# Kernel tuning notes

Hardware: AMD Instinct MI355X
Metric: run time of the kernel (lower is better)

## Reference

```python
import jax, jax.numpy as jnp
import numpy as np

B, N, C, H = 4, 2048, 384, 8
HD = C // H  # 48; divisible by 6 so RoPE3D splits into three even-sized chunks
ROPE_BASE = 100.0  # RoPE3D(100)


def _rope1d(x, p):
    # x: [B,H,N,d], p: [B,N] integer positions
    d = x.shape[-1]
    inv = 1.0 / (ROPE_BASE ** (jnp.arange(0, d, 2, dtype=jnp.float32) / d))  # [d/2]
    ang = p[:, None, :, None].astype(jnp.float32) * inv                      # [B,1,N,d/2]
    ang = jnp.concatenate([ang, ang], axis=-1)                               # [B,1,N,d]
    cos, sin = jnp.cos(ang), jnp.sin(ang)
    x1, x2 = jnp.split(x, 2, axis=-1)
    return x * cos + jnp.concatenate([-x2, x1], axis=-1) * sin


def _rope3d(x, pos):
    # x: [B,H,N,D], pos: [B,N,3]; rotate each D/3 chunk by one spatial axis
    parts = jnp.split(x, 3, axis=-1)
    return jnp.concatenate([_rope1d(parts[i], pos[..., i]) for i in range(3)], axis=-1)


def setup_inputs() -> dict:
    key = jax.random.key(0)
    ks = jax.random.split(key, 9)
    T = B * N
    s = 1.0 / np.sqrt(C).astype(np.float32)
    offs = jnp.arange(1, B + 1, dtype=jnp.int32) * N  # equal-length segments
    return {
        "query": jax.random.normal(ks[0], (T, C), jnp.float32),
        "key": jax.random.normal(ks[1], (T, C), jnp.float32),
        "value": jax.random.normal(ks[2], (T, C), jnp.float32),
        "Wq": jax.random.normal(ks[3], (C, C), jnp.float32) * s,
        "bq": jnp.zeros((C,), jnp.float32),
        "Wk": jax.random.normal(ks[4], (C, C), jnp.float32) * s,
        "bk": jnp.zeros((C,), jnp.float32),
        "Wv": jax.random.normal(ks[5], (C, C), jnp.float32) * s,
        "bv": jnp.zeros((C,), jnp.float32),
        "Wo": jax.random.normal(ks[6], (C, C), jnp.float32) * s,
        "bo": jnp.zeros((C,), jnp.float32),
        "qpos": jax.random.randint(ks[7], (T, 3), 0, 100),
        "kpos": jax.random.randint(ks[8], (T, 3), 0, 100),
        "src_point_offset": offs,
        "tgt_point_offset": offs,
    }


def reference(query, key, value, Wq, bq, Wk, bk, Wv, bv, Wo, bo,
              qpos, kpos, src_point_offset, tgt_point_offset):
    # Equal-length segments (offsets = [N,2N,...]) => the per-item python loop
    # in forward_pcd_to_pcd is exactly one batched attention over [B,N,C].
    qb = query.reshape(B, N, C)
    kb = key.reshape(B, N, C)
    vb = value.reshape(B, N, C)
    q = (qb @ Wq.T + bq).reshape(B, N, H, HD).transpose(0, 2, 1, 3)  # [B,H,N,HD]
    k = (kb @ Wk.T + bk).reshape(B, N, H, HD).transpose(0, 2, 1, 3)
    v = (vb @ Wv.T + bv).reshape(B, N, H, HD).transpose(0, 2, 1, 3)
    q = _rope3d(q, qpos.reshape(B, N, 3))
    k = _rope3d(k, kpos.reshape(B, N, 3))
    scale = 1.0 / np.sqrt(HD).astype(np.float32)
    attn = jax.nn.softmax(jnp.einsum("bhqd,bhkd->bhqk", q, k) * scale, axis=-1)
    x = jnp.einsum("bhqk,bhkd->bhqd", attn, v)  # [B,H,N,HD]
    x = x.transpose(0, 2, 1, 3).reshape(B * N, C)
    return x @ Wo.T + bo
```

## Files before the change

### kernel.cpp

```cpp
#include <hip/hip_runtime.h>
#include <hip/hip_bf16.h>
#include <math.h>


typedef __attribute__((ext_vector_type(8))) short bf16x8;
typedef __attribute__((ext_vector_type(4))) float f32x4;
typedef __attribute__((ext_vector_type(4))) short s16x4;

__device__ inline short f2bf(float f) {
    unsigned u = __float_as_uint(f);
    u += 0x7fffu + ((u >> 16) & 1u);
    return (short)(u >> 16);
}
__device__ inline unsigned pk_bf16(float a, float b) {
    __hip_bfloat162 h = __float22bfloat162_rn(make_float2(a, b));
    return *(reinterpret_cast<unsigned*>(&h));
}
__device__ inline unsigned pk2(float lo, float hi) {
    return (__float_as_uint(lo) >> 16) | (__float_as_uint(hi) & 0xffff0000u);
}
__device__ inline float bflo(unsigned u) { return __uint_as_float(u << 16); }
__device__ inline float bfhi(unsigned u) { return __uint_as_float(u & 0xffff0000u); }
__device__ inline float exp2f_fast(float x) {
#if __has_builtin(__builtin_amdgcn_exp2f)
    return __builtin_amdgcn_exp2f(x);
#else
    return exp2f(x);
#endif
}
__device__ inline float ffract(float x) {
    float r;
    asm("v_fract_f32 %0, %1" : "=v"(r) : "v"(x));
    return r;
}
__device__ inline float fsin(float x) {
    float r;
    asm("v_sin_f32 %0, %1\n\ts_nop 1" : "=v"(r) : "v"(x));
    return r;
}
__device__ inline float fcos(float x) {
    float r;
    asm("v_cos_f32 %0, %1\n\ts_nop 1" : "=v"(r) : "v"(x));
    return r;
}
__device__ inline int div48(int c) { return (c * 683) >> 15; }

__global__ __launch_bounds__(256)
void cvt_w(const float* __restrict__ w0, const float* __restrict__ w1,
           const float* __restrict__ w2, const float* __restrict__ w3,
           short* __restrict__ Wh, short* __restrict__ Wl)
{
    const float* s = blockIdx.y == 0 ? w0 : blockIdx.y == 1 ? w1
                   : blockIdx.y == 2 ? w2 : w3;
    const size_t base = (size_t)blockIdx.y * 147456;
    const size_t i = (size_t)(blockIdx.x * 256 + threadIdx.x) * 4;
    const float4 x = *(const float4*)(s + i);
    const unsigned h01 = pk2(x.x, x.y);
    const unsigned h23 = pk2(x.z, x.w);
    uint2 hv; hv.x = h01; hv.y = h23;
    uint2 lv;
    lv.x = pk2(x.x - bflo(h01), x.y - bfhi(h01));
    lv.y = pk2(x.z - bflo(h23), x.w - bfhi(h23));
    *(uint2*)(Wh + base + i) = hv;
    *(uint2*)(Wl + base + i) = lv;
}

__global__ __launch_bounds__(256)
void gemm_qkv(const float* __restrict__ q_in, const float* __restrict__ k_in,
              const float* __restrict__ v_in,
              const short* __restrict__ Whp, const short* __restrict__ Wlp,
              const float* __restrict__ bq, const float* __restrict__ bk,
              const float* __restrict__ bv,
              const int* __restrict__ qpos, const int* __restrict__ kpos,
              short* __restrict__ qp0, short* __restrict__ qtb,
              short* __restrict__ kp0, short* __restrict__ ktb,
              short* __restrict__ vp)
{
    __shared__ short Wls[2][128 * 40];

    const int z = blockIdx.z;
    const float* A = z == 0 ? q_in : z == 1 ? k_in : v_in;
    const short* Wh = Whp + (size_t)z * 147456;
    const short* Wl = Wlp + (size_t)z * 147456;
    const float* bias = z == 0 ? bq : z == 1 ? bk : bv;

    const int tid = threadIdx.x;
    const int wv = tid >> 6, lane = tid & 63;
    const int l15 = lane & 15, quad = lane >> 4;
    const int mb = blockIdx.x * 64 + (wv & 1) * 32;
    const int nbl = (wv >> 1) * 64;
    const int n0 = blockIdx.y * 128;

    const int srow = tid >> 1;
    const int sh = (tid & 1) * 16;
    const short* wg_h = Wh + (size_t)(n0 + srow) * 384 + sh;
    const short* wg_l = Wl + (size_t)(n0 + srow) * 384 + sh;
    short* ds_h = &Wls[0][srow * 40 + sh];
    short* ds_l = &Wls[1][srow * 40 + sh];

    f32x4 acc[2][4] = {};
    const float* a0 = A + (size_t)(mb + l15) * 384 + quad * 8;

    for (int ks = 0; ks < 12; ++ks) {
        const int o = ks * 32;
        __syncthreads();
        *(bf16x8*)(ds_h)     = *(const bf16x8*)(wg_h + o);
        *(bf16x8*)(ds_h + 8) = *(const bf16x8*)(wg_h + o + 8);
        *(bf16x8*)(ds_l)     = *(const bf16x8*)(wg_l + o);
        *(bf16x8*)(ds_l + 8) = *(const bf16x8*)(wg_l + o + 8);
        bf16x8 ah[2], al[2];
        #pragma unroll
        for (int mt = 0; mt < 2; ++mt) {
            const float4 x0 = *(const float4*)(a0 + o + mt * 16 * 384);
            const float4 x1 = *(const float4*)(a0 + o + mt * 16 * 384 + 4);
            union { bf16x8 v; unsigned u[4]; } ch, cl;
            ch.u[0] = pk2(x0.x, x0.y);
            ch.u[1] = pk2(x0.z, x0.w);
            ch.u[2] = pk2(x1.x, x1.y);
            ch.u[3] = pk2(x1.z, x1.w);
            cl.u[0] = pk2(x0.x - bflo(ch.u[0]), x0.y - bfhi(ch.u[0]));
            cl.u[1] = pk2(x0.z - bflo(ch.u[1]), x0.w - bfhi(ch.u[1]));
            cl.u[2] = pk2(x1.x - bflo(ch.u[2]), x1.y - bfhi(ch.u[2]));
            cl.u[3] = pk2(x1.z - bflo(ch.u[3]), x1.w - bfhi(ch.u[3]));
            ah[mt] = ch.v;
            al[mt] = cl.v;
        }
        __syncthreads();

        #pragma unroll
        for (int nt = 0; nt < 4; ++nt) {
            const int wr = (nbl + nt * 16 + l15) * 40 + quad * 8;
            const bf16x8 wh = *(const bf16x8*)&Wls[0][wr];
            const bf16x8 wl = *(const bf16x8*)&Wls[1][wr];
            #pragma unroll
            for (int mt = 0; mt < 2; ++mt) {
                acc[mt][nt] = __builtin_amdgcn_mfma_f32_16x16x32_bf16(
                    ah[mt], wh, acc[mt][nt], 0, 0, 0);
                acc[mt][nt] = __builtin_amdgcn_mfma_f32_16x16x32_bf16(
                    al[mt], wh, acc[mt][nt], 0, 0, 0);
                acc[mt][nt] = __builtin_amdgcn_mfma_f32_16x16x32_bf16(
                    ah[mt], wl, acc[mt][nt], 0, 0, 0);
            }
        }
    }

    if (z < 2) {
        const int* pos = z ? kpos : qpos;
        const float oscale = z ? 1.0f : 0.2082339551542919f;
        const float invf = exp2f_fast(-(float)(l15 & 7) * 0.8304820237218405f)
                         * 0.15915494309189535f;
        const bool lo_half = (l15 < 8);
        #pragma unroll
        for (int nt = 0; nt < 4; ++nt) {
            const int c = n0 + nbl + nt * 16 + l15;
            const int h = div48(c);
            const int r0 = c - h * 48;
            const int axis = r0 >> 4;
            const float bb = bias[c];
            #pragma unroll
            for (int mt = 0; mt < 2; ++mt) {
                float a[4], pr[4];
                #pragma unroll
                for (int r = 0; r < 4; ++r) a[r] = acc[mt][nt][r] + bb;
                #pragma unroll
                for (int r = 0; r < 4; ++r) pr[r] = __shfl_xor(a[r], 8);
                #pragma unroll
                for (int r = 0; r < 4; ++r) {
                    const int t = mb + mt * 16 + quad * 4 + r;
                    const float pp = (float)pos[t * 3 + axis];
                    const float fr = ffract(pp * invf);
                    const float sn = fsin(fr), cn = fcos(fr);
                    const float o2 = lo_half ? (a[r] * cn - pr[r] * sn)
                                             : (a[r] * cn + pr[r] * sn);
                    const short val = f2bf(o2 * oscale);
                    const int b = t >> 11, n = t & 2047;
                    const int bh_ = b * 8 + h;
                    if (r0 < 32) {
                        short* pbuf = z ? kp0 : qp0;
                        pbuf[(((size_t)bh_ * 128 + (n >> 4)) * 64
                              + (r0 >> 3) * 16 + (n & 15)) * 8 + (r0 & 7)] = val;
                    } else if (z == 0) {
                        const int dd = r0 - 32;
                        qtb[(((size_t)bh_ * 128 + (n >> 4)) * 32
                             + (dd >> 3) * 16 + (n & 15)) * 8 + (dd & 7)] = val;
                    } else {
                        const int dd = r0 - 32;
                        ktb[(((size_t)bh_ * 64 + (n >> 5)) * 64
                             + ((n >> 4) & 1) * 32 + (dd >> 3) * 16 + (n & 15)) * 8
                            + (dd & 7)] = val;
                    }
                }
            }
        }
    } else {
        #pragma unroll
        for (int nt = 0; nt < 4; ++nt) {
            const int c = n0 + nbl + nt * 16 + l15;
            const int h = div48(c);
            const int r0 = c - h * 48;
            const float bb = bias[c];
            #pragma unroll
            for (int mt = 0; mt < 2; ++mt) {
                const int t0 = mb + mt * 16 + quad * 4;
                const int b = t0 >> 11, n = t0 & 2047;
                const int bh_ = b * 8 + h;
                s16x4 pk;
                #pragma unroll
                for (int r = 0; r < 4; ++r)
                    ((short*)&pk)[r] = f2bf(acc[mt][nt][r] + bb);
                const size_t off =
                    ((((size_t)bh_ * 16 + (n >> 7)) * 3 + (r0 >> 4)) * 4
                     + ((n >> 5) & 3)) * 512
                    + (((n >> 3) & 3) * 16 + (r0 & 15)) * 8 + (n & 7);
                *(s16x4*)(vp + off) = pk;
            }
        }
    }
}

__global__ __launch_bounds__(256)
void gemm_out(const short* __restrict__ xh, const short* __restrict__ xl,
              const short* __restrict__ Whp, const short* __restrict__ Wlp,
              const float* __restrict__ bo, float* __restrict__ out)
{
    __shared__ short Wls[2][128 * 40];

    const short* Wh = Whp + (size_t)3 * 147456;
    const short* Wl = Wlp + (size_t)3 * 147456;

    const int tid = threadIdx.x;
    const int wv = tid >> 6, lane = tid & 63;
    const int l15 = lane & 15, quad = lane >> 4;
    const int mb = blockIdx.x * 64 + (wv & 1) * 32;
    const int nbl = (wv >> 1) * 64;
    const int n0 = blockIdx.y * 128;

    const int srow = tid >> 1;
    const int sh = (tid & 1) * 16;
    const short* wg_h = Wh + (size_t)(n0 + srow) * 384 + sh;
    const short* wg_l = Wl + (size_t)(n0 + srow) * 384 + sh;
    short* ds_h = &Wls[0][srow * 40 + sh];
    short* ds_l = &Wls[1][srow * 40 + sh];

    f32x4 acc[2][4] = {};
    const short* a0 = xh + (size_t)(mb + l15) * 384 + quad * 8;
    const short* a1 = xl + (size_t)(mb + l15) * 384 + quad * 8;

    for (int ks = 0; ks < 12; ++ks) {
        const int o = ks * 32;
        __syncthreads();
        *(bf16x8*)(ds_h)     = *(const bf16x8*)(wg_h + o);
        *(bf16x8*)(ds_h + 8) = *(const bf16x8*)(wg_h + o + 8);
        *(bf16x8*)(ds_l)     = *(const bf16x8*)(wg_l + o);
        *(bf16x8*)(ds_l + 8) = *(const bf16x8*)(wg_l + o + 8);
        bf16x8 ah[2], al[2];
        #pragma unroll
        for (int mt = 0; mt < 2; ++mt) {
            ah[mt] = *(const bf16x8*)(a0 + o + mt * 16 * 384);
            al[mt] = *(const bf16x8*)(a1 + o + mt * 16 * 384);
        }
        __syncthreads();

        #pragma unroll
        for (int nt = 0; nt < 4; ++nt) {
            const int wr = (nbl + nt * 16 + l15) * 40 + quad * 8;
            const bf16x8 wh = *(const bf16x8*)&Wls[0][wr];
            const bf16x8 wl = *(const bf16x8*)&Wls[1][wr];
            #pragma unroll
            for (int mt = 0; mt < 2; ++mt) {
                acc[mt][nt] = __builtin_amdgcn_mfma_f32_16x16x32_bf16(
                    ah[mt], wh, acc[mt][nt], 0, 0, 0);
                acc[mt][nt] = __builtin_amdgcn_mfma_f32_16x16x32_bf16(
                    al[mt], wh, acc[mt][nt], 0, 0, 0);
                acc[mt][nt] = __builtin_amdgcn_mfma_f32_16x16x32_bf16(
                    ah[mt], wl, acc[mt][nt], 0, 0, 0);
            }
        }
    }

    #pragma unroll
    for (int nt = 0; nt < 4; ++nt) {
        const int c = n0 + nbl + nt * 16 + l15;
        const float bb = bo[c];
        #pragma unroll
        for (int mt = 0; mt < 2; ++mt)
            #pragma unroll
            for (int r = 0; r < 4; ++r)
                out[(size_t)(mb + mt * 16 + quad * 4 + r) * 384 + c] =
                    acc[mt][nt][r] + bb;
    }
}

__global__ __launch_bounds__(256, 4)
void attn_mfma(const short* __restrict__ Qp0, const short* __restrict__ Qt,
               const short* __restrict__ Kp0, const short* __restrict__ Kt,
               const short* __restrict__ Vp,
               short* __restrict__ x2h, short* __restrict__ x2l)
{
    __shared__ short Ps[4][16][136];
    const int tid = threadIdx.x;
    const int wave = tid >> 6;
    const int lane = tid & 63;
    const int l15 = lane & 15;
    const int quad = lane >> 4;
    const int L = blockIdx.x;
    const int bh = (L & 7) + ((L >> 8) << 3);
    const int q0 = ((L >> 3) & 31) << 6;

    const int qt16 = (q0 >> 4) + wave;
    const bf16x8 qb0 = *(const bf16x8*)
        (Qp0 + (((size_t)bh * 128 + qt16) * 64 + lane) * 8);
    const bf16x8 qtl = *(const bf16x8*)
        (Qt + (((size_t)bh * 128 + qt16) * 32 + (lane & 31)) * 8);
    const bf16x8 z8 = {0, 0, 0, 0, 0, 0, 0, 0};
    const bf16x8 qb1lo = (quad < 2) ? qtl : z8;
    const bf16x8 qb1hi = (quad < 2) ? z8 : qtl;

    f32x4 of[3];
    #pragma unroll
    for (int t = 0; t < 3; ++t) of[t] = (f32x4){0.f, 0.f, 0.f, 0.f};
    f32x4 lsv = (f32x4){0.f, 0.f, 0.f, 0.f};

    for (int kt = 0; kt < 16; ++kt) {
        const short* kb = Kp0 + (((size_t)bh * 128 + kt * 8) * 64 + lane) * 8;
        const short* kq = Kt + (((size_t)bh * 64 + kt * 4) * 64 + lane) * 8;

        const short* vb = Vp + (((size_t)bh * 16 + kt) * 12 * 64 + lane) * 8;
        bf16x8 va[12];
        #pragma unroll
        for (int i = 0; i < 12; ++i)
            va[i] = *(const bf16x8*)(vb + i * 512);

        f32x4 sf[8];
        #pragma unroll
        for (int p = 0; p < 4; ++p) {
            const bf16x8 ka0 = *(const bf16x8*)(kb + (2 * p) * 512);
            const bf16x8 ka1 = *(const bf16x8*)(kb + (2 * p + 1) * 512);
            const bf16x8 kts = *(const bf16x8*)(kq + p * 512);
            f32x4 z0 = (f32x4){0.f, 0.f, 0.f, 0.f};
            z0 = __builtin_amdgcn_mfma_f32_16x16x32_bf16(ka0, qb0, z0, 0, 0, 0);
            sf[2 * p] = __builtin_amdgcn_mfma_f32_16x16x32_bf16(kts, qb1lo, z0, 0, 0, 0);
            f32x4 z1 = (f32x4){0.f, 0.f, 0.f, 0.f};
            z1 = __builtin_amdgcn_mfma_f32_16x16x32_bf16(ka1, qb0, z1, 0, 0, 0);
            sf[2 * p + 1] = __builtin_amdgcn_mfma_f32_16x16x32_bf16(kts, qb1hi, z1, 0, 0, 0);
        }

        #pragma unroll
        for (int t = 0; t < 8; ++t) {
            const float p0 = exp2f_fast(sf[t][0]);
            const float p1 = exp2f_fast(sf[t][1]);
            const float p2 = exp2f_fast(sf[t][2]);
            const float p3 = exp2f_fast(sf[t][3]);
            lsv[0] += p0; lsv[1] += p1; lsv[2] += p2; lsv[3] += p3;
            uint2 w;
            w.x = pk_bf16(p0, p1);
            w.y = pk_bf16(p2, p3);
            *(uint2*)&Ps[wave][l15][t * 16 + quad * 4] = w;
        }

        bf16x8 pb[4];
        #pragma unroll
        for (int s = 0; s < 4; ++s)
            pb[s] = *(const bf16x8*)&Ps[wave][l15][s * 32 + quad * 8];
        #pragma unroll
        for (int t = 0; t < 3; ++t) {
            #pragma unroll
            for (int s = 0; s < 4; ++s) {
                of[t] = __builtin_amdgcn_mfma_f32_16x16x32_bf16(
                    va[t * 4 + s], pb[s], of[t], 0, 0, 0);
            }
        }
    }

    float ls = (lsv[0] + lsv[1]) + (lsv[2] + lsv[3]);
    ls += __shfl_xor(ls, 16);
    ls += __shfl_xor(ls, 32);
    const float invl = 1.0f / ls;
    const int b = bh >> 3, h = bh & 7;
    const size_t off = (size_t)(b * 2048 + q0 + wave * 16 + l15) * 384
                     + h * 48 + quad * 4;
    #pragma unroll
    for (int t = 0; t < 3; ++t) {
        const float o0 = of[t][0] * invl;
        const float o1 = of[t][1] * invl;
        const float o2 = of[t][2] * invl;
        const float o3 = of[t][3] * invl;
        const unsigned h01 = pk_bf16(o0, o1);
        const unsigned h23 = pk_bf16(o2, o3);
        uint2 hv; hv.x = h01; hv.y = h23;
        uint2 lv;
        lv.x = pk2(o0 - bflo(h01), o1 - bfhi(h01));
        lv.y = pk2(o2 - bflo(h23), o3 - bfhi(h23));
        *(uint2*)(x2h + off + t * 16) = hv;
        *(uint2*)(x2l + off + t * 16) = lv;
    }
}

extern "C" void kernel_launch(void* const* d_in, const int* in_sizes, int n_in,
                              void* d_out, int out_size, void* d_ws, size_t ws_size,
                              hipStream_t stream)
{
    const float* query = (const float*)d_in[0];
    const float* key_  = (const float*)d_in[1];
    const float* value = (const float*)d_in[2];
    const float* Wq = (const float*)d_in[3];
    const float* bq = (const float*)d_in[4];
    const float* Wk = (const float*)d_in[5];
    const float* bk = (const float*)d_in[6];
    const float* Wv = (const float*)d_in[7];
    const float* bv = (const float*)d_in[8];
    const float* Wo = (const float*)d_in[9];
    const float* bo = (const float*)d_in[10];
    const int* qpos = (const int*)d_in[11];
    const int* kpos = (const int*)d_in[12];

    const size_t QP0_S = (size_t)32 * 128 * 64 * 8;
    const size_t QT_S  = (size_t)32 * 128 * 32 * 8;
    const size_t KP0_S = QP0_S;
    const size_t KT_S  = (size_t)32 * 64 * 64 * 8;
    const size_t VP_S  = (size_t)32 * 16 * 12 * 64 * 8;
    const size_t X2_S  = (size_t)8192 * 384;
    const size_t W_S   = (size_t)4 * 384 * 384;

    short* w = (short*)d_ws;
    short* qp0 = w;  w += QP0_S;
    short* qtb = w;  w += QT_S;
    short* kp0 = w;  w += KP0_S;
    short* ktb = w;  w += KT_S;
    short* vp  = w;  w += VP_S;
    short* x2h = w;  w += X2_S;
    short* x2l = w;  w += X2_S;
    short* Wh  = w;  w += W_S;
    short* Wl  = w;

    const dim3 blk(256);
    cvt_w<<<dim3(144, 4), blk, 0, stream>>>(Wq, Wk, Wv, Wo, Wh, Wl);
    gemm_qkv<<<dim3(128, 3, 3), blk, 0, stream>>>(
        query, key_, value, Wh, Wl, bq, bk, bv, qpos, kpos,
        qp0, qtb, kp0, ktb, vp);
    attn_mfma<<<dim3(1024), blk, 0, stream>>>(qp0, qtb, kp0, ktb, vp, x2h, x2l);
    gemm_out<<<dim3(128, 3), blk, 0, stream>>>(x2h, x2l, Wh, Wl, bo,
                                               (float*)d_out);
}
```

Measured before the change: 226.9 us.

## Pre-tile weights into MFMA fragment layout and load directly from global

The weight conversion kernel now writes the bf16 hi/lo weights in a layout that matches the MFMA B-fragment order per 16-column tile and 32-wide k-step. The QKV and output GEMMs then read each lane's 8-element fragment with one contiguous global load, so the shared-memory staging and the two barriers per k-step are gone. Launch bounds are raised to request more resident blocks per CU. The cost is that weight fragments are no longer shared through LDS: each wave re-reads its own fragments from global or L2, and any latency there is now exposed inside the MFMA loop.

New measurement: 235.2 us. 3.6% more time.

```diff
diff --git a/kernel.cpp b/kernel.cpp
--- a/kernel.cpp
+++ b/kernel.cpp
@@ -52,20 +52,24 @@
 {
     const float* s = blockIdx.y == 0 ? w0 : blockIdx.y == 1 ? w1
                    : blockIdx.y == 2 ? w2 : w3;
-    const size_t base = (size_t)blockIdx.y * 147456;
     const size_t i = (size_t)(blockIdx.x * 256 + threadIdx.x) * 4;
+    const int c = (int)(i / 384);
+    const int k = (int)(i % 384);
     const float4 x = *(const float4*)(s + i);
     const unsigned h01 = pk2(x.x, x.y);
     const unsigned h23 = pk2(x.z, x.w);
+    const unsigned l01 = pk2(x.x - bflo(h01), x.y - bfhi(h01));
+    const unsigned l23 = pk2(x.z - bflo(h23), x.w - bfhi(h23));
+    const size_t off =
+        ((((size_t)blockIdx.y * 24 + (c >> 4)) * 12 + (k >> 5)) * 64
+         + ((k >> 3) & 3) * 16 + (c & 15)) * 8 + (k & 7);
     uint2 hv; hv.x = h01; hv.y = h23;
-    uint2 lv;
-    lv.x = pk2(x.x - bflo(h01), x.y - bfhi(h01));
-    lv.y = pk2(x.z - bflo(h23), x.w - bfhi(h23));
-    *(uint2*)(Wh + base + i) = hv;
-    *(uint2*)(Wl + base + i) = lv;
-}
-
-__global__ __launch_bounds__(256)
+    uint2 lv; lv.x = l01; lv.y = l23;
+    *(uint2*)(Wh + off) = hv;
+    *(uint2*)(Wl + off) = lv;
+}
+
+__global__ __launch_bounds__(256, 4)
 void gemm_qkv(const float* __restrict__ q_in, const float* __restrict__ k_in,
               const float* __restrict__ v_in,
               const short* __restrict__ Whp, const short* __restrict__ Wlp,
@@ -76,12 +80,8 @@
               short* __restrict__ kp0, short* __restrict__ ktb,
               short* __restrict__ vp)
 {
-    __shared__ short Wls[2][128 * 40];
-
     const int z = blockIdx.z;
     const float* A = z == 0 ? q_in : z == 1 ? k_in : v_in;
-    const short* Wh = Whp + (size_t)z * 147456;
-    const short* Wl = Wlp + (size_t)z * 147456;
     const float* bias = z == 0 ? bq : z == 1 ? bk : bv;
 
     const int tid = threadIdx.x;
@@ -91,23 +91,15 @@
     const int nbl = (wv >> 1) * 64;
     const int n0 = blockIdx.y * 128;
 
-    const int srow = tid >> 1;
-    const int sh = (tid & 1) * 16;
-    const short* wg_h = Wh + (size_t)(n0 + srow) * 384 + sh;
-    const short* wg_l = Wl + (size_t)(n0 + srow) * 384 + sh;
-    short* ds_h = &Wls[0][srow * 40 + sh];
-    short* ds_l = &Wls[1][srow * 40 + sh];
+    const int tbase = (size_t)blockIdx.y * 8 + (wv >> 1) * 4 + z * 24;
+    const short* wfh = Whp + ((size_t)tbase * 12 * 64 + lane) * 8;
+    const short* wfl = Wlp + ((size_t)tbase * 12 * 64 + lane) * 8;
 
     f32x4 acc[2][4] = {};
     const float* a0 = A + (size_t)(mb + l15) * 384 + quad * 8;
 
     for (int ks = 0; ks < 12; ++ks) {
         const int o = ks * 32;
-        __syncthreads();
-        *(bf16x8*)(ds_h)     = *(const bf16x8*)(wg_h + o);
-        *(bf16x8*)(ds_h + 8) = *(const bf16x8*)(wg_h + o + 8);
-        *(bf16x8*)(ds_l)     = *(const bf16x8*)(wg_l + o);
-        *(bf16x8*)(ds_l + 8) = *(const bf16x8*)(wg_l + o + 8);
         bf16x8 ah[2], al[2];
         #pragma unroll
         for (int mt = 0; mt < 2; ++mt) {
@@ -125,13 +117,11 @@
             ah[mt] = ch.v;
             al[mt] = cl.v;
         }
-        __syncthreads();
 
         #pragma unroll
         for (int nt = 0; nt < 4; ++nt) {
-            const int wr = (nbl + nt * 16 + l15) * 40 + quad * 8;
-            const bf16x8 wh = *(const bf16x8*)&Wls[0][wr];
-            const bf16x8 wl = *(const bf16x8*)&Wls[1][wr];
+            const bf16x8 wh = *(const bf16x8*)(wfh + (nt * 12 + ks) * 512);
+            const bf16x8 wl = *(const bf16x8*)(wfl + (nt * 12 + ks) * 512);
             #pragma unroll
             for (int mt = 0; mt < 2; ++mt) {
                 acc[mt][nt] = __builtin_amdgcn_mfma_f32_16x16x32_bf16(
@@ -218,16 +208,11 @@
     }
 }
 
-__global__ __launch_bounds__(256)
+__global__ __launch_bounds__(256, 4)
 void gemm_out(const short* __restrict__ xh, const short* __restrict__ xl,
               const short* __restrict__ Whp, const short* __restrict__ Wlp,
               const float* __restrict__ bo, float* __restrict__ out)
 {
-    __shared__ short Wls[2][128 * 40];
-
-    const short* Wh = Whp + (size_t)3 * 147456;
-    const short* Wl = Wlp + (size_t)3 * 147456;
-
     const int tid = threadIdx.x;
     const int wv = tid >> 6, lane = tid & 63;
     const int l15 = lane & 15, quad = lane >> 4;
@@ -235,12 +220,9 @@
     const int nbl = (wv >> 1) * 64;
     const int n0 = blockIdx.y * 128;
 
-    const int srow = tid >> 1;
-    const int sh = (tid & 1) * 16;
-    const short* wg_h = Wh + (size_t)(n0 + srow) * 384 + sh;
-    const short* wg_l = Wl + (size_t)(n0 + srow) * 384 + sh;
-    short* ds_h = &Wls[0][srow * 40 + sh];
-    short* ds_l = &Wls[1][srow * 40 + sh];
+    const int tbase = (size_t)blockIdx.y * 8 + (wv >> 1) * 4 + 3 * 24;
+    const short* wfh = Whp + ((size_t)tbase * 12 * 64 + lane) * 8;
+    const short* wfl = Wlp + ((size_t)tbase * 12 * 64 + lane) * 8;
 
     f32x4 acc[2][4] = {};
     const short* a0 = xh + (size_t)(mb + l15) * 384 + quad * 8;
@@ -248,24 +230,17 @@
 
     for (int ks = 0; ks < 12; ++ks) {
         const int o = ks * 32;
-        __syncthreads();
-        *(bf16x8*)(ds_h)     = *(const bf16x8*)(wg_h + o);
-        *(bf16x8*)(ds_h + 8) = *(const bf16x8*)(wg_h + o + 8);
-        *(bf16x8*)(ds_l)     = *(const bf16x8*)(wg_l + o);
-        *(bf16x8*)(ds_l + 8) = *(const bf16x8*)(wg_l + o + 8);
         bf16x8 ah[2], al[2];
         #pragma unroll
         for (int mt = 0; mt < 2; ++mt) {
             ah[mt] = *(const bf16x8*)(a0 + o + mt * 16 * 384);
             al[mt] = *(const bf16x8*)(a1 + o + mt * 16 * 384);
         }
-        __syncthreads();
 
         #pragma unroll
         for (int nt = 0; nt < 4; ++nt) {
-            const int wr = (nbl + nt * 16 + l15) * 40 + quad * 8;
-            const bf16x8 wh = *(const bf16x8*)&Wls[0][wr];
-            const bf16x8 wl = *(const bf16x8*)&Wls[1][wr];
+            const bf16x8 wh = *(const bf16x8*)(wfh + (nt * 12 + ks) * 512);
+            const bf16x8 wl = *(const bf16x8*)(wfl + (nt * 12 + ks) * 512);
             #pragma unroll
             for (int mt = 0; mt < 2; ++mt) {
                 acc[mt][nt] = __builtin_amdgcn_mfma_f32_16x16x32_bf16(
```
